# Performance work log

Measured on AMD Instinct MI355X. Metric: run time of the kernel, lower is better.

## Reference

```python
import jax, jax.numpy as jnp
import numpy as np

B, T, D = 512, 512, 256          # batch, timesteps, input feature dim
H0, H1, H2, H3 = 32, 64, 64, 64  # VanillaRNN, LSTM, LSTM, GRU hidden sizes
NC = 12                          # num_cumulants


def setup_inputs() -> dict:
    key = jax.random.key(0)
    ks = jax.random.split(key, 12)
    f32 = jnp.float32

    def w(k, shape, fan_in):
        return jax.random.normal(k, shape, f32) * f32(1.0 / np.sqrt(fan_in))

    inp = {}
    inp["pixels_observation"] = jax.random.normal(ks[0], (B, T, D), f32)
    # VanillaRNN(32): input_to_hidden Linear(D->32), hidden_to_hidden Linear(32->32), both with bias
    inp["van_wi"] = w(ks[1], (D, H0), D)
    inp["van_bi"] = jnp.zeros((H0,), f32)
    inp["van_wh"] = w(ks[2], (H0, H0), H0)
    inp["van_bh"] = jnp.zeros((H0,), f32)
    # LSTM(64) on 32-dim input: Linear(32+64 -> 4*64)
    inp["lstm1_w"] = w(ks[3], (H0 + H1, 4 * H1), H0 + H1)
    inp["lstm1_b"] = jnp.zeros((4 * H1,), f32)
    # LSTM(64) on 64-dim input
    inp["lstm2_w"] = w(ks[4], (H1 + H2, 4 * H2), H1 + H2)
    inp["lstm2_b"] = jnp.zeros((4 * H2,), f32)
    # GRU(64)
    inp["gru_wi"] = w(ks[5], (H2, 3 * H3), H2)
    inp["gru_wh"] = w(ks[6], (H3, 3 * H3), H3)
    inp["gru_b"] = jnp.zeros((3 * H3,), f32)
    # MLP (32, 32, 12)
    inp["mlp_w1"] = w(ks[7], (H3, 32), H3)
    inp["mlp_b1"] = jnp.zeros((32,), f32)
    inp["mlp_w2"] = w(ks[8], (32, 32), 32)
    inp["mlp_b2"] = jnp.zeros((32,), f32)
    inp["mlp_w3"] = w(ks[9], (32, NC), 32)
    inp["mlp_b3"] = jnp.zeros((NC,), f32)
    # learned successor_features parameter (preference_vectors = ones(NC,1) constant)
    inp["successor_features"] = jax.random.normal(ks[10], (NC, 1), f32)
    inp["action_index"] = 0
    return inp


def _lstm_step(x, h, c, w, b):
    # haiku LSTM: gates on concat([x, h]); split order i, g, f, o; forget bias +1
    gated = jnp.concatenate([x, h], axis=-1) @ w + b
    i, g, f, o = jnp.split(gated, 4, axis=-1)
    c = jax.nn.sigmoid(f + 1.0) * c + jax.nn.sigmoid(i) * jnp.tanh(g)
    h = jax.nn.sigmoid(o) * jnp.tanh(c)
    return h, c


def reference(pixels_observation, van_wi, van_bi, van_wh, van_bh,
              lstm1_w, lstm1_b, lstm2_w, lstm2_b,
              gru_wi, gru_wh, gru_b,
              mlp_w1, mlp_b1, mlp_w2, mlp_b2, mlp_w3, mlp_b3,
              successor_features, action_index):
    assert action_index == 0  # source selects branch with a static Python int
    x = pixels_observation
    Bsz = x.shape[0]
    f32 = x.dtype

    def step(carry, x_t):
        h0, h1, c1, h2, c2, h3 = carry
        # VanillaRNN: relu(Wi x + bi + Wh h + bh)
        h0 = jax.nn.relu(x_t @ van_wi + van_bi + h0 @ van_wh + van_bh)
        h1, c1 = _lstm_step(h0, h1, c1, lstm1_w, lstm1_b)
        h2, c2 = _lstm_step(h1, h2, c2, lstm2_w, lstm2_b)
        # haiku GRU
        gates_x = h2 @ gru_wi                       # [B, 3H]
        zr_x, a_x = gates_x[:, :2 * H3], gates_x[:, 2 * H3:]
        zr = zr_x + h3 @ gru_wh[:, :2 * H3] + gru_b[:2 * H3]
        z, r = jnp.split(jax.nn.sigmoid(zr), 2, axis=-1)
        a = jnp.tanh(a_x + (r * h3) @ gru_wh[:, 2 * H3:] + gru_b[2 * H3:])
        h3 = (1.0 - z) * h3 + z * a
        return (h0, h1, c1, h2, c2, h3), None

    init = (jnp.zeros((Bsz, H0), f32),
            jnp.zeros((Bsz, H1), f32), jnp.zeros((Bsz, H1), f32),
            jnp.zeros((Bsz, H2), f32), jnp.zeros((Bsz, H2), f32),
            jnp.zeros((Bsz, H3), f32))
    carry, _ = jax.lax.scan(step, init, jnp.swapaxes(x, 0, 1))  # time-major scan
    emb = carry[-1]  # final GRU output = DeepRNN output at last timestep

    # MLP (32, 32, NC): relu on hidden layers, linear final layer
    emb = jax.nn.relu(emb @ mlp_w1 + mlp_b1)
    emb = jax.nn.relu(emb @ mlp_w2 + mlp_b2)
    emb = emb @ mlp_w3 + mlp_b3                     # [B, NC]

    preference_vectors = jnp.ones((NC, 1), f32)
    # einsum('ca,bc->ba', pref * succ, emb)
    policy_params = emb @ (preference_vectors * successor_features)  # [B, 1]
    return successor_features, preference_vectors, policy_params
```

## Files before the change

### kernel.cpp

```cpp
#include <hip/hip_runtime.h>
#include <stdint.h>

#define Tsz 512
#define Dsz 256

#define R_VAN 0
#define R_L1A 1
#define R_L1B 2
#define R_L2A 3
#define R_L2B 4
#define R_GX  5
#define R_GR0 6
#define R_GR1 7

union UHp { uint32_t u; _Float16 s[2]; };
__device__ __forceinline__ uint32_t packh(float a, float b) {
    UHp x; x.s[0] = (_Float16)a; x.s[1] = (_Float16)b; return x.u;
}
__device__ __forceinline__ float dot2(uint32_t w, uint32_t a, float c) {
#if __has_builtin(__builtin_amdgcn_fdot2)
    typedef _Float16 h2 __attribute__((ext_vector_type(2)));
    union U { uint32_t u; h2 h; };
    U W, A; W.u = w; A.u = a;
    return __builtin_amdgcn_fdot2(W.h, A.h, c, false);
#else
    float d;
    asm("v_dot2_f32_f16 %0, %1, %2, %3" : "=v"(d) : "v"(w), "v"(a), "v"(c));
    return d;
#endif
}

__device__ __forceinline__ float fexp2(float x) {
#if __has_builtin(__builtin_amdgcn_exp2f)
    return __builtin_amdgcn_exp2f(x);
#else
    return exp2f(x);
#endif
}
__device__ __forceinline__ float frcp(float x) {
#if __has_builtin(__builtin_amdgcn_rcpf)
    return __builtin_amdgcn_rcpf(x);
#else
    return 1.0f / x;
#endif
}
#define LOG2E 1.44269504f
__device__ __forceinline__ float fsig(float x)  { return frcp(1.0f + fexp2(-LOG2E * x)); }
__device__ __forceinline__ float ftanh(float x) { return 2.0f * frcp(1.0f + fexp2(-2.0f * LOG2E * x)) - 1.0f; }

#define D4(ACC, WP, V) \
    do { ACC = dot2((WP)[0], (V).x, ACC); ACC = dot2((WP)[1], (V).y, ACC); \
         ACC = dot2((WP)[2], (V).z, ACC); ACC = dot2((WP)[3], (V).w, ACC); } while (0)
#define D4X(A, X, WP, V) \
    do { A = dot2((WP)[0], (V).x, A); X = dot2((WP)[1], (V).y, X); \
         A = dot2((WP)[2], (V).z, A); X = dot2((WP)[3], (V).w, X); } while (0)

#define WAITGE(cache, ridx, need) \
    do { if ((cache) < (need)) { \
        volatile const int* _pf = (volatile const int*)&prog[(ridx)]; \
        int _v = *_pf; \
        while (_v < (need)) _v = *_pf; \
        (cache) = _v; } } while (0)

#define SIGNAL(ridx, val) \
    do { asm volatile("s_waitcnt lgkmcnt(0)" ::: "memory"); \
         *((volatile int*)&prog[(ridx)]) = (val); } while (0)

__global__ __attribute__((amdgpu_flat_work_group_size(512, 512),
                          amdgpu_waves_per_eu(2, 2)))
void rnn_flag2(
    const float* __restrict__ pix,
    const float* __restrict__ van_wi, const float* __restrict__ van_bi,
    const float* __restrict__ van_wh, const float* __restrict__ van_bh,
    const float* __restrict__ w1g, const float* __restrict__ b1g,
    const float* __restrict__ w2g, const float* __restrict__ b2g,
    const float* __restrict__ gwi, const float* __restrict__ gwh,
    const float* __restrict__ gb,
    const float* __restrict__ mw1, const float* __restrict__ mb1,
    const float* __restrict__ mw2, const float* __restrict__ mb2,
    const float* __restrict__ mw3, const float* __restrict__ mb3,
    const float* __restrict__ sf,
    float* __restrict__ out)
{
    const int tid  = threadIdx.x;
    const int wv   = tid >> 6;
    const int lane = tid & 63;
    const int r0   = 2 * blockIdx.x;

    int role;
    switch (wv) {
        case 0: role = R_L2A; break;
        case 1: role = R_L2B; break;
        case 2: role = R_VAN; break;
        case 3: role = R_GX;  break;
        case 4: role = R_GR0; break;
        case 5: role = R_GR1; break;
        case 6: role = R_L1A; break;
        default: role = R_L1B; break;
    }

    __shared__ __align__(16) _Float16 xb [4][2][256];
    __shared__ __align__(16) _Float16 h0b[4][2][32];
    __shared__ __align__(16) _Float16 h1b[4][2][64];
    __shared__ __align__(16) _Float16 h2b[4][2][64];
    __shared__ __align__(16) _Float16 gxb[4][2][192];
    __shared__ __align__(16) _Float16 h3s[2][64];
    __shared__ __align__(16) _Float16 rh3s[2][64];
    __shared__ int prog[8];
    __shared__ float sHf[2][64];
    __shared__ float sT[2][64];
    __shared__ float sP[2][12];

    uint32_t wreg[128];
    float bz0 = 0.f, bz1 = 0.f, bz2 = 0.f;
    float st0 = 0.f, st1 = 0.f;
    float4 pxA0{}, pxB0{}, pxA1{}, pxB1{};
    const float* pr0 = nullptr; const float* pr1 = nullptr;

    if (role == R_VAN) {
        const int c = lane & 31, s = lane >> 5;
#pragma unroll
        for (int j = 0; j < 64; ++j)
            wreg[j] = packh(van_wi[(128 * s + 2 * j) * 32 + c],
                            van_wi[(128 * s + 2 * j + 1) * 32 + c]);
#pragma unroll
        for (int j = 0; j < 8; ++j)
            wreg[64 + j] = packh(van_wh[(16 * s + 2 * j) * 32 + c],
                                 van_wh[(16 * s + 2 * j + 1) * 32 + c]);
        bz0 = van_bi[c] + van_bh[c];
        pr0 = pix + (size_t)r0 * Tsz * Dsz;
        pr1 = pr0 + (size_t)Tsz * Dsz;
#pragma unroll
        for (int t = 0; t < 2; ++t) {
            float4 p0 = *(const float4*)(pr0 + (size_t)t * Dsz + 4 * lane);
            float4 p1 = *(const float4*)(pr1 + (size_t)t * Dsz + 4 * lane);
            uint32_t* x0 = (uint32_t*)xb[t][0];
            uint32_t* x1 = (uint32_t*)xb[t][1];
            x0[2 * lane] = packh(p0.x, p0.y); x0[2 * lane + 1] = packh(p0.z, p0.w);
            x1[2 * lane] = packh(p1.x, p1.y); x1[2 * lane + 1] = packh(p1.z, p1.w);
        }
        pxA0 = *(const float4*)(pr0 + 2 * (size_t)Dsz + 4 * lane);
        pxA1 = *(const float4*)(pr1 + 2 * (size_t)Dsz + 4 * lane);
        pxB0 = *(const float4*)(pr0 + 3 * (size_t)Dsz + 4 * lane);
        pxB1 = *(const float4*)(pr1 + 3 * (size_t)Dsz + 4 * lane);
    } else if (role == R_L1A || role == R_L1B) {
        const int p = (role == R_L1A ? 0 : 64) + lane;
        const int u = p >> 1, odd = p & 1;
        const int c0 = odd ? 128 + u : u, c1 = c0 + 64;
#pragma unroll
        for (int j = 0; j < 48; ++j)
            wreg[j] = packh(w1g[(2 * j) * 256 + c0], w1g[(2 * j + 1) * 256 + c0]);
#pragma unroll
        for (int j = 0; j < 48; ++j)
            wreg[48 + j] = packh(w1g[(2 * j) * 256 + c1], w1g[(2 * j + 1) * 256 + c1]);
        bz0 = b1g[c0]; bz1 = b1g[c1];
    } else if (role == R_L2A || role == R_L2B) {
        const int p = (role == R_L2A ? 0 : 64) + lane;
        const int u = p >> 1, odd = p & 1;
        const int c0 = odd ? 128 + u : u, c1 = c0 + 64;
#pragma unroll
        for (int j = 0; j < 64; ++j)
            wreg[j] = packh(w2g[(2 * j) * 256 + c0], w2g[(2 * j + 1) * 256 + c0]);
#pragma unroll
        for (int j = 0; j < 64; ++j)
            wreg[64 + j] = packh(w2g[(2 * j) * 256 + c1], w2g[(2 * j + 1) * 256 + c1]);
        bz0 = b2g[c0]; bz1 = b2g[c1];
    } else if (role == R_GX) {
#pragma unroll
        for (int j = 0; j < 32; ++j) {
            wreg[j]      = packh(gwi[(2 * j) * 192 + lane],       gwi[(2 * j + 1) * 192 + lane]);
            wreg[32 + j] = packh(gwi[(2 * j) * 192 + 64 + lane],  gwi[(2 * j + 1) * 192 + 64 + lane]);
            wreg[64 + j] = packh(gwi[(2 * j) * 192 + 128 + lane], gwi[(2 * j + 1) * 192 + 128 + lane]);
        }
        bz0 = gb[lane]; bz1 = gb[64 + lane]; bz2 = gb[128 + lane];
    } else {
#pragma unroll
        for (int j = 0; j < 32; ++j) {
            wreg[j]      = packh(gwh[(2 * j) * 192 + lane],       gwh[(2 * j + 1) * 192 + lane]);
            wreg[32 + j] = packh(gwh[(2 * j) * 192 + 64 + lane],  gwh[(2 * j + 1) * 192 + 64 + lane]);
            wreg[64 + j] = packh(gwh[(2 * j) * 192 + 128 + lane], gwh[(2 * j + 1) * 192 + 128 + lane]);
        }
    }

    for (int i = tid; i < 4 * 2 * 32;  i += 512) ((_Float16*)h0b)[i] = (_Float16)0.f;
    for (int i = tid; i < 4 * 2 * 64;  i += 512) ((_Float16*)h1b)[i] = (_Float16)0.f;
    for (int i = tid; i < 4 * 2 * 64;  i += 512) ((_Float16*)h2b)[i] = (_Float16)0.f;
    for (int i = tid; i < 4 * 2 * 192; i += 512) ((_Float16*)gxb)[i] = (_Float16)0.f;
    for (int i = tid; i < 2 * 64; i += 512) { ((_Float16*)h3s)[i] = (_Float16)0.f; ((_Float16*)rh3s)[i] = (_Float16)0.f; }
    if (tid < 8) prog[tid] = 0;
    __syncthreads();

    if (role == R_VAN) {
        const int c = lane & 31, s = lane >> 5;
        int cA = 0, cB = 0;
        for (int t = 0; t < Tsz; ++t) {
            WAITGE(cA, R_L1A, t - 3);
            WAITGE(cB, R_L1B, t - 3);
            if (t + 2 < Tsz) {
                uint32_t* x0 = (uint32_t*)xb[(t + 2) & 3][0];
                uint32_t* x1 = (uint32_t*)xb[(t + 2) & 3][1];
                x0[2 * lane] = packh(pxA0.x, pxA0.y); x0[2 * lane + 1] = packh(pxA0.z, pxA0.w);
                x1[2 * lane] = packh(pxA1.x, pxA1.y); x1[2 * lane + 1] = packh(pxA1.z, pxA1.w);
            }
            pxA0 = pxB0; pxA1 = pxB1;
            if (t + 4 < Tsz) {
                pxB0 = *(const float4*)(pr0 + (size_t)(t + 4) * Dsz + 4 * lane);
                pxB1 = *(const float4*)(pr1 + (size_t)(t + 4) * Dsz + 4 * lane);
            }
#pragma unroll
            for (int r = 0; r < 2; ++r) {
                const uint4* xq = ((const uint4*)xb[t & 3][r]) + 16 * s;
                const uint4* hq = ((const uint4*)h0b[(t - 1) & 3][r]) + 2 * s;
                float a0 = 0.f, a1 = 0.f;
#pragma unroll
                for (int q = 0; q < 16; q += 2) {
                    uint4 v0 = xq[q], v1 = xq[q + 1];
                    D4(a0, &wreg[4 * q], v0);
                    D4(a1, &wreg[4 * q + 4], v1);
                }
                {
                    uint4 v0 = hq[0], v1 = hq[1];
                    D4(a0, &wreg[64], v0);
                    D4(a1, &wreg[68], v1);
                }
                float acc = a0 + a1;
                acc += __shfl_xor(acc, 32);
                if (s == 0) h0b[t & 3][r][c] = (_Float16)fmaxf(acc + bz0, 0.f);
            }
            SIGNAL(R_VAN, t + 1);
        }
    } else if (role == R_L1A || role == R_L1B) {
        const int prt = (role == R_L1A) ? R_L1B : R_L1A;
        const int p = (role == R_L1A ? 0 : 64) + lane;
        const int u = p >> 1, odd = p & 1;
        int cv = 0, cp = 0, c2a = 0, c2b = 0;
        for (int t = 0; t < Tsz; ++t) {
            WAITGE(cv, R_VAN, t + 1);
            WAITGE(cp, prt, t);
            WAITGE(c2a, R_L2A, t - 3);
            WAITGE(c2b, R_L2B, t - 3);
#pragma unroll
            for (int r = 0; r < 2; ++r) {
                const uint4* aq = (const uint4*)h0b[t & 3][r];
                const uint4* bq = (const uint4*)h1b[(t - 1) & 3][r];
                float a0 = bz0, a1 = bz1, x0 = 0.f, x1 = 0.f;
#pragma unroll
                for (int q = 0; q < 4; ++q) {
                    uint4 v = aq[q];
                    D4X(a0, x0, &wreg[4 * q], v);
                    D4X(a1, x1, &wreg[48 + 4 * q], v);
                }
#pragma unroll
                for (int q = 0; q < 8; ++q) {
                    uint4 v = bq[q];
                    D4X(a0, x0, &wreg[16 + 4 * q], v);
                    D4X(a1, x1, &wreg[64 + 4 * q], v);
                }
                float g0 = a0 + x0, g1 = a1 + x1;
                float ain = odd ? g0 + 1.f : g0;
                float bin = odd ? g1 : g1 + g1;
                float s0 = fsig(ain);
                float s1 = fsig(bin);
                float send = s0 * (2.f * s1 - 1.f);
                float prx = __shfl_xor(send, 1);
                float cs = r ? st1 : st0;
                cs = s0 * cs + prx;
                if (r) st1 = cs; else st0 = cs;
                float tc = ftanh(cs);
                if (odd) h1b[t & 3][r][u] = (_Float16)(s1 * tc);
            }
            SIGNAL(role, t + 1);
        }
    } else if (role == R_L2A || role == R_L2B) {
        const int prt = (role == R_L2A) ? R_L2B : R_L2A;
        const int p = (role == R_L2A ? 0 : 64) + lane;
        const int u = p >> 1, odd = p & 1;
        int c1a = 0, c1b = 0, cp = 0, cg = 0;
        for (int t = 0; t < Tsz; ++t) {
            WAITGE(c1a, R_L1A, t + 1);
            WAITGE(c1b, R_L1B, t + 1);
            WAITGE(cp, prt, t);
            WAITGE(cg, R_GX, t - 3);
#pragma unroll
            for (int r = 0; r < 2; ++r) {
                const uint4* aq = (const uint4*)h1b[t & 3][r];
                const uint4* bq = (const uint4*)h2b[(t - 1) & 3][r];
                float a0 = bz0, a1 = bz1, x0 = 0.f, x1 = 0.f;
#pragma unroll
                for (int q = 0; q < 8; ++q) {
                    uint4 v = aq[q];
                    D4X(a0, x0, &wreg[4 * q], v);
                    D4X(a1, x1, &wreg[64 + 4 * q], v);
                }
#pragma unroll
                for (int q = 0; q < 8; ++q) {
                    uint4 v = bq[q];
                    D4X(a0, x0, &wreg[32 + 4 * q], v);
                    D4X(a1, x1, &wreg[96 + 4 * q], v);
                }
                float g0 = a0 + x0, g1 = a1 + x1;
                float ain = odd ? g0 + 1.f : g0;
                float bin = odd ? g1 : g1 + g1;
                float s0 = fsig(ain);
                float s1 = fsig(bin);
                float send = s0 * (2.f * s1 - 1.f);
                float prx = __shfl_xor(send, 1);
                float cs = r ? st1 : st0;
                cs = s0 * cs + prx;
                if (r) st1 = cs; else st0 = cs;
                float tc = ftanh(cs);
                if (odd) h2b[t & 3][r][u] = (_Float16)(s1 * tc);
            }
            SIGNAL(role, t + 1);
        }
    } else if (role == R_GX) {
        int c2a = 0, c2b = 0, g0c = 0, g1c = 0;
        for (int t = 0; t < Tsz; ++t) {
            WAITGE(c2a, R_L2A, t + 1);
            WAITGE(c2b, R_L2B, t + 1);
            WAITGE(g0c, R_GR0, t - 3);
            WAITGE(g1c, R_GR1, t - 3);
#pragma unroll
            for (int r = 0; r < 2; ++r) {
                const uint4* hq = (const uint4*)h2b[t & 3][r];
                float az = bz0, ar = bz1, aa = bz2;
#pragma unroll
                for (int q = 0; q < 8; ++q) {
                    uint4 v = hq[q];
                    D4(az, &wreg[4 * q], v);
                    D4(ar, &wreg[32 + 4 * q], v);
                    D4(aa, &wreg[64 + 4 * q], v);
                }
                gxb[t & 3][r][lane]       = (_Float16)az;
                gxb[t & 3][r][64 + lane]  = (_Float16)ar;
                gxb[t & 3][r][128 + lane] = (_Float16)aa;
            }
            SIGNAL(R_GX, t + 1);
        }
    } else {
        const int r = (role == R_GR0) ? 0 : 1;
        int cg = 0;
        for (int t = 0; t < Tsz; ++t) {
            WAITGE(cg, R_GX, t + 1);
            const uint4* hq = (const uint4*)h3s[r];
            float az = (float)gxb[t & 3][r][lane];
            float ar = (float)gxb[t & 3][r][64 + lane];
#pragma unroll
            for (int q = 0; q < 8; ++q) {
                uint4 v = hq[q];
                D4(az, &wreg[4 * q], v);
                D4(ar, &wreg[32 + 4 * q], v);
            }
            float z = fsig(az);
            rh3s[r][lane] = (_Float16)(fsig(ar) * st0);
            float ga = (float)gxb[t & 3][r][128 + lane];
            asm volatile("s_waitcnt lgkmcnt(0)" ::: "memory");
            const uint4* rq = (const uint4*)rh3s[r];
            float aa = ga, ab = 0.f;
#pragma unroll
            for (int q = 0; q < 8; ++q) {
                uint4 v = rq[q];
                if (q & 1) { D4(ab, &wreg[64 + 4 * q], v); }
                else       { D4(aa, &wreg[64 + 4 * q], v); }
            }
            float av = ftanh(aa + ab);
            st0 = (1.f - z) * st0 + z * av;
            h3s[r][lane] = (_Float16)st0;
            SIGNAL(role, t + 1);
        }
    }

    if (role == R_GR0) sHf[0][lane] = st0;
    if (role == R_GR1) sHf[1][lane] = st0;
    __syncthreads();

    if (tid < 64) {
        const int r = tid >> 5, c = tid & 31;
        float acc = mb1[c];
#pragma unroll
        for (int kk = 0; kk < 64; ++kk) acc = fmaf(sHf[r][kk], mw1[kk * 32 + c], acc);
        sT[r][c] = fmaxf(acc, 0.f);
    }
    __syncthreads();
    if (tid < 64) {
        const int r = tid >> 5, c = tid & 31;
        float acc = mb2[c];
#pragma unroll
        for (int kk = 0; kk < 32; ++kk) acc = fmaf(sT[r][kk], mw2[kk * 32 + c], acc);
        sT[r][32 + c] = fmaxf(acc, 0.f);
    }
    __syncthreads();
    if (tid < 24) {
        const int r = tid / 12, c = tid - 12 * r;
        float acc = mb3[c];
#pragma unroll
        for (int kk = 0; kk < 32; ++kk) acc = fmaf(sT[r][32 + kk], mw3[kk * 12 + c], acc);
        sP[r][c] = acc;
    }
    __syncthreads();
    if (tid < 2) {
        float acc = 0.f;
#pragma unroll
        for (int kk = 0; kk < 12; ++kk) acc = fmaf(sP[tid][kk], sf[kk], acc);
        out[24 + r0 + tid] = acc;
    }
    if (blockIdx.x == 0 && tid < 12) {
        out[tid] = sf[tid];
        out[12 + tid] = 1.0f;
    }
}

extern "C" void kernel_launch(void* const* d_in, const int* in_sizes, int n_in,
                              void* d_out, int out_size, void* d_ws, size_t ws_size,
                              hipStream_t stream) {
    (void)in_sizes; (void)n_in; (void)d_ws; (void)ws_size; (void)out_size;
    const float* pix    = (const float*)d_in[0];
    const float* van_wi = (const float*)d_in[1];
    const float* van_bi = (const float*)d_in[2];
    const float* van_wh = (const float*)d_in[3];
    const float* van_bh = (const float*)d_in[4];
    const float* w1     = (const float*)d_in[5];
    const float* b1     = (const float*)d_in[6];
    const float* w2     = (const float*)d_in[7];
    const float* b2     = (const float*)d_in[8];
    const float* gwi    = (const float*)d_in[9];
    const float* gwh    = (const float*)d_in[10];
    const float* gb     = (const float*)d_in[11];
    const float* mw1    = (const float*)d_in[12];
    const float* mb1    = (const float*)d_in[13];
    const float* mw2    = (const float*)d_in[14];
    const float* mb2    = (const float*)d_in[15];
    const float* mw3    = (const float*)d_in[16];
    const float* mb3    = (const float*)d_in[17];
    const float* sf     = (const float*)d_in[18];
    float* out = (float*)d_out;

    rnn_flag2<<<256, 512, 0, stream>>>(
        pix, van_wi, van_bi, van_wh, van_bh,
        w1, b1, w2, b2, gwi, gwh, gb,
        mw1, mb1, mw2, mb2, mw3, mb3, sf, out);
}
```

Before: 655.3 us.

## Split each pipeline stage into per-row waves with per-row progress flags

Each block previously ran 8 waves where every stage wave handled both batch rows in sequence. Now 14 waves are launched (896 threads), one set of stage waves per batch row, each with its own progress flag, so the two rows' recurrences run concurrently instead of serially within a wave. This shortens the per-timestep critical path of each stage. In exchange it doubles the weight registers held per block and raises occupancy demands (waves_per_eu 4), which risks register pressure and more contention on the SIMDs.

```diff
diff --git a/kernel.cpp b/kernel.cpp
--- a/kernel.cpp
+++ b/kernel.cpp
@@ -4,14 +4,13 @@
 #define Tsz 512
 #define Dsz 256
 
-#define R_VAN 0
-#define R_L1A 1
-#define R_L1B 2
-#define R_L2A 3
-#define R_L2B 4
-#define R_GX  5
-#define R_GR0 6
-#define R_GR1 7
+#define P_VAN(row) ((row) * 7 + 0)
+#define P_L1A(row) ((row) * 7 + 1)
+#define P_L1B(row) ((row) * 7 + 2)
+#define P_L2A(row) ((row) * 7 + 3)
+#define P_L2B(row) ((row) * 7 + 4)
+#define P_GX(row)  ((row) * 7 + 5)
+#define P_GR(row)  ((row) * 7 + 6)
 
 union UHp { uint32_t u; _Float16 s[2]; };
 __device__ __forceinline__ uint32_t packh(float a, float b) {
@@ -66,9 +65,9 @@
     do { asm volatile("s_waitcnt lgkmcnt(0)" ::: "memory"); \
          *((volatile int*)&prog[(ridx)]) = (val); } while (0)
 
-__global__ __attribute__((amdgpu_flat_work_group_size(512, 512),
-                          amdgpu_waves_per_eu(2, 2)))
-void rnn_flag2(
+__global__ __attribute__((amdgpu_flat_work_group_size(896, 896),
+                          amdgpu_waves_per_eu(4, 4)))
+void rnn_rs(
     const float* __restrict__ pix,
     const float* __restrict__ van_wi, const float* __restrict__ van_bi,
     const float* __restrict__ van_wh, const float* __restrict__ van_bh,
@@ -87,16 +86,22 @@
     const int lane = tid & 63;
     const int r0   = 2 * blockIdx.x;
 
-    int role;
+    int kind, row, half = 0;
     switch (wv) {
-        case 0: role = R_L2A; break;
-        case 1: role = R_L2B; break;
-        case 2: role = R_VAN; break;
-        case 3: role = R_GX;  break;
-        case 4: role = R_GR0; break;
-        case 5: role = R_GR1; break;
-        case 6: role = R_L1A; break;
-        default: role = R_L1B; break;
+        case 0:  kind = 2; row = 0; half = 0; break;
+        case 1:  kind = 2; row = 0; half = 1; break;
+        case 2:  kind = 2; row = 1; half = 0; break;
+        case 3:  kind = 2; row = 1; half = 1; break;
+        case 4:  kind = 1; row = 0; half = 0; break;
+        case 5:  kind = 1; row = 0; half = 1; break;
+        case 6:  kind = 1; row = 1; half = 0; break;
+        case 7:  kind = 1; row = 1; half = 1; break;
+        case 8:  kind = 0; row = 0; break;
+        case 9:  kind = 0; row = 1; break;
+        case 10: kind = 3; row = 0; break;
+        case 11: kind = 3; row = 1; break;
+        case 12: kind = 4; row = 0; break;
+        default: kind = 4; row = 1; break;
     }
 
     __shared__ __align__(16) _Float16 xb [4][2][256];
@@ -106,18 +111,18 @@
     __shared__ __align__(16) _Float16 gxb[4][2][192];
     __shared__ __align__(16) _Float16 h3s[2][64];
     __shared__ __align__(16) _Float16 rh3s[2][64];
-    __shared__ int prog[8];
+    __shared__ int prog[14];
     __shared__ float sHf[2][64];
     __shared__ float sT[2][64];
     __shared__ float sP[2][12];
 
     uint32_t wreg[128];
     float bz0 = 0.f, bz1 = 0.f, bz2 = 0.f;
-    float st0 = 0.f, st1 = 0.f;
-    float4 pxA0{}, pxB0{}, pxA1{}, pxB1{};
-    const float* pr0 = nullptr; const float* pr1 = nullptr;
-
-    if (role == R_VAN) {
+    float st0 = 0.f;
+    float4 pxA{}, pxB{};
+    const float* pr = nullptr;
+
+    if (kind == 0) {
         const int c = lane & 31, s = lane >> 5;
 #pragma unroll
         for (int j = 0; j < 64; ++j)
@@ -128,23 +133,17 @@
             wreg[64 + j] = packh(van_wh[(16 * s + 2 * j) * 32 + c],
                                  van_wh[(16 * s + 2 * j + 1) * 32 + c]);
         bz0 = van_bi[c] + van_bh[c];
-        pr0 = pix + (size_t)r0 * Tsz * Dsz;
-        pr1 = pr0 + (size_t)Tsz * Dsz;
+        pr = pix + (size_t)(r0 + row) * Tsz * Dsz;
 #pragma unroll
         for (int t = 0; t < 2; ++t) {
-            float4 p0 = *(const float4*)(pr0 + (size_t)t * Dsz + 4 * lane);
-            float4 p1 = *(const float4*)(pr1 + (size_t)t * Dsz + 4 * lane);
-            uint32_t* x0 = (uint32_t*)xb[t][0];
-            uint32_t* x1 = (uint32_t*)xb[t][1];
+            float4 p0 = *(const float4*)(pr + (size_t)t * Dsz + 4 * lane);
+            uint32_t* x0 = (uint32_t*)xb[t][row];
             x0[2 * lane] = packh(p0.x, p0.y); x0[2 * lane + 1] = packh(p0.z, p0.w);
-            x1[2 * lane] = packh(p1.x, p1.y); x1[2 * lane + 1] = packh(p1.z, p1.w);
-        }
-        pxA0 = *(const float4*)(pr0 + 2 * (size_t)Dsz + 4 * lane);
-        pxA1 = *(const float4*)(pr1 + 2 * (size_t)Dsz + 4 * lane);
-        pxB0 = *(const float4*)(pr0 + 3 * (size_t)Dsz + 4 * lane);
-        pxB1 = *(const float4*)(pr1 + 3 * (size_t)Dsz + 4 * lane);
-    } else if (role == R_L1A || role == R_L1B) {
-        const int p = (role == R_L1A ? 0 : 64) + lane;
+        }
+        pxA = *(const float4*)(pr + 2 * (size_t)Dsz + 4 * lane);
+        pxB = *(const float4*)(pr + 3 * (size_t)Dsz + 4 * lane);
+    } else if (kind == 1) {
+        const int p = half * 64 + lane;
         const int u = p >> 1, odd = p & 1;
         const int c0 = odd ? 128 + u : u, c1 = c0 + 64;
 #pragma unroll
@@ -154,8 +153,8 @@
         for (int j = 0; j < 48; ++j)
             wreg[48 + j] = packh(w1g[(2 * j) * 256 + c1], w1g[(2 * j + 1) * 256 + c1]);
         bz0 = b1g[c0]; bz1 = b1g[c1];
-    } else if (role == R_L2A || role == R_L2B) {
-        const int p = (role == R_L2A ? 0 : 64) + lane;
+    } else if (kind == 2) {
+        const int p = half * 64 + lane;
         const int u = p >> 1, odd = p & 1;
         const int c0 = odd ? 128 + u : u, c1 = c0 + 64;
 #pragma unroll
@@ -165,7 +164,7 @@
         for (int j = 0; j < 64; ++j)
             wreg[64 + j] = packh(w2g[(2 * j) * 256 + c1], w2g[(2 * j + 1) * 256 + c1]);
         bz0 = b2g[c0]; bz1 = b2g[c1];
-    } else if (role == R_GX) {
+    } else if (kind == 3) {
 #pragma unroll
         for (int j = 0; j < 32; ++j) {
             wreg[j]      = packh(gwi[(2 * j) * 192 + lane],       gwi[(2 * j + 1) * 192 + lane]);
@@ -182,35 +181,30 @@
         }
     }
 
-    for (int i = tid; i < 4 * 2 * 32;  i += 512) ((_Float16*)h0b)[i] = (_Float16)0.f;
-    for (int i = tid; i < 4 * 2 * 64;  i += 512) ((_Float16*)h1b)[i] = (_Float16)0.f;
-    for (int i = tid; i < 4 * 2 * 64;  i += 512) ((_Float16*)h2b)[i] = (_Float16)0.f;
-    for (int i = tid; i < 4 * 2 * 192; i += 512) ((_Float16*)gxb)[i] = (_Float16)0.f;
-    for (int i = tid; i < 2 * 64; i += 512) { ((_Float16*)h3s)[i] = (_Float16)0.f; ((_Float16*)rh3s)[i] = (_Float16)0.f; }
-    if (tid < 8) prog[tid] = 0;
+    for (int i = tid; i < 4 * 2 * 32;  i += 896) ((_Float16*)h0b)[i] = (_Float16)0.f;
+    for (int i = tid; i < 4 * 2 * 64;  i += 896) ((_Float16*)h1b)[i] = (_Float16)0.f;
+    for (int i = tid; i < 4 * 2 * 64;  i += 896) ((_Float16*)h2b)[i] = (_Float16)0.f;
+    for (int i = tid; i < 4 * 2 * 192; i += 896) ((_Float16*)gxb)[i] = (_Float16)0.f;
+    for (int i = tid; i < 2 * 64; i += 896) { ((_Float16*)h3s)[i] = (_Float16)0.f; ((_Float16*)rh3s)[i] = (_Float16)0.f; }
+    if (tid < 14) prog[tid] = 0;
     __syncthreads();
 
-    if (role == R_VAN) {
+    if (kind == 0) {
         const int c = lane & 31, s = lane >> 5;
         int cA = 0, cB = 0;
         for (int t = 0; t < Tsz; ++t) {
-            WAITGE(cA, R_L1A, t - 3);
-            WAITGE(cB, R_L1B, t - 3);
+            WAITGE(cA, P_L1A(row), t - 3);
+            WAITGE(cB, P_L1B(row), t - 3);
             if (t + 2 < Tsz) {
-                uint32_t* x0 = (uint32_t*)xb[(t + 2) & 3][0];
-                uint32_t* x1 = (uint32_t*)xb[(t + 2) & 3][1];
-                x0[2 * lane] = packh(pxA0.x, pxA0.y); x0[2 * lane + 1] = packh(pxA0.z, pxA0.w);
-                x1[2 * lane] = packh(pxA1.x, pxA1.y); x1[2 * lane + 1] = packh(pxA1.z, pxA1.w);
-            }
-            pxA0 = pxB0; pxA1 = pxB1;
-            if (t + 4 < Tsz) {
-                pxB0 = *(const float4*)(pr0 + (size_t)(t + 4) * Dsz + 4 * lane);
-                pxB1 = *(const float4*)(pr1 + (size_t)(t + 4) * Dsz + 4 * lane);
-            }
-#pragma unroll
-            for (int r = 0; r < 2; ++r) {
-                const uint4* xq = ((const uint4*)xb[t & 3][r]) + 16 * s;
-                const uint4* hq = ((const uint4*)h0b[(t - 1) & 3][r]) + 2 * s;
+                uint32_t* x0 = (uint32_t*)xb[(t + 2) & 3][row];
+                x0[2 * lane] = packh(pxA.x, pxA.y); x0[2 * lane + 1] = packh(pxA.z, pxA.w);
+            }
+            pxA = pxB;
+            if (t + 4 < Tsz)
+                pxB = *(const float4*)(pr + (size_t)(t + 4) * Dsz + 4 * lane);
+            {
+                const uint4* xq = ((const uint4*)xb[t & 3][row]) + 16 * s;
+                const uint4* hq = ((const uint4*)h0b[(t - 1) & 3][row]) + 2 * s;
                 float a0 = 0.f, a1 = 0.f;
 #pragma unroll
                 for (int q = 0; q < 16; q += 2) {
@@ -225,24 +219,24 @@
                 }
                 float acc = a0 + a1;
                 acc += __shfl_xor(acc, 32);
-                if (s == 0) h0b[t & 3][r][c] = (_Float16)fmaxf(acc + bz0, 0.f);
-            }
-            SIGNAL(R_VAN, t + 1);
-        }
-    } else if (role == R_L1A || role == R_L1B) {
-        const int prt = (role == R_L1A) ? R_L1B : R_L1A;
-        const int p = (role == R_L1A ? 0 : 64) + lane;
+                if (s == 0) h0b[t & 3][row][c] = (_Float16)fmaxf(acc + bz0, 0.f);
+            }
+            SIGNAL(P_VAN(row), t + 1);
+        }
+    } else if (kind == 1) {
+        const int self = half ? P_L1B(row) : P_L1A(row);
+        const int prt  = half ? P_L1A(row) : P_L1B(row);
+        const int p = half * 64 + lane;
         const int u = p >> 1, odd = p & 1;
         int cv = 0, cp = 0, c2a = 0, c2b = 0;
         for (int t = 0; t < Tsz; ++t) {
-            WAITGE(cv, R_VAN, t + 1);
+            WAITGE(cv, P_VAN(row), t + 1);
             WAITGE(cp, prt, t);
-            WAITGE(c2a, R_L2A, t - 3);
-            WAITGE(c2b, R_L2B, t - 3);
-#pragma unroll
-            for (int r = 0; r < 2; ++r) {
-                const uint4* aq = (const uint4*)h0b[t & 3][r];
-                const uint4* bq = (const uint4*)h1b[(t - 1) & 3][r];
+            WAITGE(c2a, P_L2A(row), t - 3);
+            WAITGE(c2b, P_L2B(row), t - 3);
+            {
+                const uint4* aq = (const uint4*)h0b[t & 3][row];
+                const uint4* bq = (const uint4*)h1b[(t - 1) & 3][row];
                 float a0 = bz0, a1 = bz1, x0 = 0.f, x1 = 0.f;
 #pragma unroll
                 for (int q = 0; q < 4; ++q) {
@@ -263,28 +257,26 @@
                 float s1 = fsig(bin);
                 float send = s0 * (2.f * s1 - 1.f);
                 float prx = __shfl_xor(send, 1);
-                float cs = r ? st1 : st0;
-                cs = s0 * cs + prx;
-                if (r) st1 = cs; else st0 = cs;
-                float tc = ftanh(cs);
-                if (odd) h1b[t & 3][r][u] = (_Float16)(s1 * tc);
-            }
-            SIGNAL(role, t + 1);
-        }
-    } else if (role == R_L2A || role == R_L2B) {
-        const int prt = (role == R_L2A) ? R_L2B : R_L2A;
-        const int p = (role == R_L2A ? 0 : 64) + lane;
+                st0 = s0 * st0 + prx;
+                float tc = ftanh(st0);
+                if (odd) h1b[t & 3][row][u] = (_Float16)(s1 * tc);
+            }
+            SIGNAL(self, t + 1);
+        }
+    } else if (kind == 2) {
+        const int self = half ? P_L2B(row) : P_L2A(row);
+        const int prt  = half ? P_L2A(row) : P_L2B(row);
+        const int p = half * 64 + lane;
         const int u = p >> 1, odd = p & 1;
         int c1a = 0, c1b = 0, cp = 0, cg = 0;
         for (int t = 0; t < Tsz; ++t) {
-            WAITGE(c1a, R_L1A, t + 1);
-            WAITGE(c1b, R_L1B, t + 1);
+            WAITGE(c1a, P_L1A(row), t + 1);
+            WAITGE(c1b, P_L1B(row), t + 1);
             WAITGE(cp, prt, t);
-            WAITGE(cg, R_GX, t - 3);
-#pragma unroll
-            for (int r = 0; r < 2; ++r) {
-                const uint4* aq = (const uint4*)h1b[t & 3][r];
-                const uint4* bq = (const uint4*)h2b[(t - 1) & 3][r];
+            WAITGE(cg, P_GX(row), t - 3);
+            {
+                const uint4* aq = (const uint4*)h1b[t & 3][row];
+                const uint4* bq = (const uint4*)h2b[(t - 1) & 3][row];
                 float a0 = bz0, a1 = bz1, x0 = 0.f, x1 = 0.f;
 #pragma unroll
                 for (int q = 0; q < 8; ++q) {
@@ -305,24 +297,20 @@
                 float s1 = fsig(bin);
                 float send = s0 * (2.f * s1 - 1.f);
                 float prx = __shfl_xor(send, 1);
-                float cs = r ? st1 : st0;
-                cs = s0 * cs + prx;
-                if (r) st1 = cs; else st0 = cs;
-                float tc = ftanh(cs);
-                if (odd) h2b[t & 3][r][u] = (_Float16)(s1 * tc);
-            }
-            SIGNAL(role, t + 1);
-        }
-    } else if (role == R_GX) {
-        int c2a = 0, c2b = 0, g0c = 0, g1c = 0;
+                st0 = s0 * st0 + prx;
+                float tc = ftanh(st0);
+                if (odd) h2b[t & 3][row][u] = (_Float16)(s1 * tc);
+            }
+            SIGNAL(self, t + 1);
+        }
+    } else if (kind == 3) {
+        int c2a = 0, c2b = 0, gc = 0;
         for (int t = 0; t < Tsz; ++t) {
-            WAITGE(c2a, R_L2A, t + 1);
-            WAITGE(c2b, R_L2B, t + 1);
-            WAITGE(g0c, R_GR0, t - 3);
-            WAITGE(g1c, R_GR1, t - 3);
-#pragma unroll
-            for (int r = 0; r < 2; ++r) {
-                const uint4* hq = (const uint4*)h2b[t & 3][r];
+            WAITGE(c2a, P_L2A(row), t + 1);
+            WAITGE(c2b, P_L2B(row), t + 1);
+            WAITGE(gc, P_GR(row), t - 3);
+            {
+                const uint4* hq = (const uint4*)h2b[t & 3][row];
                 float az = bz0, ar = bz1, aa = bz2;
 #pragma unroll
                 for (int q = 0; q < 8; ++q) {
@@ -331,20 +319,19 @@
                     D4(ar, &wreg[32 + 4 * q], v);
                     D4(aa, &wreg[64 + 4 * q], v);
                 }
-                gxb[t & 3][r][lane]       = (_Float16)az;
-                gxb[t & 3][r][64 + lane]  = (_Float16)ar;
-                gxb[t & 3][r][128 + lane] = (_Float16)aa;
-            }
-            SIGNAL(R_GX, t + 1);
+                gxb[t & 3][row][lane]       = (_Float16)az;
+                gxb[t & 3][row][64 + lane]  = (_Float16)ar;
+                gxb[t & 3][row][128 + lane] = (_Float16)aa;
+            }
+            SIGNAL(P_GX(row), t + 1);
         }
     } else {
-        const int r = (role == R_GR0) ? 0 : 1;
         int cg = 0;
         for (int t = 0; t < Tsz; ++t) {
-            WAITGE(cg, R_GX, t + 1);
-            const uint4* hq = (const uint4*)h3s[r];
-            float az = (float)gxb[t & 3][r][lane];
-            float ar = (float)gxb[t & 3][r][64 + lane];
+            WAITGE(cg, P_GX(row), t + 1);
+            const uint4* hq = (const uint4*)h3s[row];
+            float az = (float)gxb[t & 3][row][lane];
+            float ar = (float)gxb[t & 3][row][64 + lane];
 #pragma unroll
             for (int q = 0; q < 8; ++q) {
                 uint4 v = hq[q];
@@ -352,10 +339,10 @@
                 D4(ar, &wreg[32 + 4 * q], v);
             }
             float z = fsig(az);
-            rh3s[r][lane] = (_Float16)(fsig(ar) * st0);
-            float ga = (float)gxb[t & 3][r][128 + lane];
+            rh3s[row][lane] = (_Float16)(fsig(ar) * st0);
+            float ga = (float)gxb[t & 3][row][128 + lane];
             asm volatile("s_waitcnt lgkmcnt(0)" ::: "memory");
-            const uint4* rq = (const uint4*)rh3s[r];
+            const uint4* rq = (const uint4*)rh3s[row];
             float aa = ga, ab = 0.f;
 #pragma unroll
             for (int q = 0; q < 8; ++q) {
@@ -365,13 +352,13 @@
             }
             float av = ftanh(aa + ab);
             st0 = (1.f - z) * st0 + z * av;
-            h3s[r][lane] = (_Float16)st0;
-            SIGNAL(role, t + 1);
-        }
-    }
-
-    if (role == R_GR0) sHf[0][lane] = st0;
-    if (role == R_GR1) sHf[1][lane] = st0;
+            h3s[row][lane] = (_Float16)st0;
+            SIGNAL(P_GR(row), t + 1);
+        }
+    }
+
+    if (wv == 12) sHf[0][lane] = st0;
+    if (wv == 13) sHf[1][lane] = st0;
     __syncthreads();
 
     if (tid < 64) {
@@ -435,7 +422,7 @@
     const float* sf     = (const float*)d_in[18];
     float* out = (float*)d_out;
 
-    rnn_flag2<<<256, 512, 0, stream>>>(
+    rnn_rs<<<256, 896, 0, stream>>>(
         pix, van_wi, van_bi, van_wh, van_bh,
         w1, b1, w2, b2, gwi, gwh, gb,
         mw1, mb1, mw2, mb2, mw3, mb3, sf, out);
```

Result: slower. 1.987 ms (+203.1%).
